# Optimization experiments

Hardware: AMD Instinct MI355X
Metric: run time of the kernel (lower is better)

## Reference

```python
import jax, jax.numpy as jnp
import numpy as np

B, N, D, H = 4, 2048, 1024, 16
HD = D // H          # head dim before LRPE doubling
CHUNK = 64
BASE = 10000.0
EPS = 1e-6


def setup_inputs() -> dict:
    key = jax.random.key(0)
    ks = jax.random.split(key, 8)
    s = 0.02
    return {
        "x": jax.random.normal(ks[0], (B, N, D), jnp.float32),
        "Wq": jax.random.normal(ks[1], (D, D), jnp.float32) * s,
        "Wk": jax.random.normal(ks[2], (D, D), jnp.float32) * s,
        "Wv": jax.random.normal(ks[3], (D, D), jnp.float32) * s,
        "Wo": jax.random.normal(ks[4], (D, D), jnp.float32) * s,
        "Wg1": jax.random.normal(ks[5], (D, H), jnp.float32) * s,
        "Wg2": jax.random.normal(ks[6], (H, D), jnp.float32) * s,
        "norm_w": jnp.ones((D,), jnp.float32),
    }


def _lrpe(x, theta):
    # cosine LRPE (lrpe_type=6): d -> 2d, concat([x*cos, x*sin])
    c = jnp.cos(theta)[None, :, None, :]
    s = jnp.sin(theta)[None, :, None, :]
    return jnp.concatenate([x * c, x * s], axis=-1)


def _chunk_gla(q, k, v, g):
    # GLA chunked scan: S_t = diag(exp(g_t)) S_{t-1} + k_t^T v_t ; o_t = q_t S_t
    # q,k,g: (b,n,h,dk), v: (b,n,h,dv)
    b, n, h, dk = q.shape
    dv = v.shape[-1]
    nc = n // CHUNK

    def to_chunks(t):
        return t.reshape(b, nc, CHUNK, t.shape[2], t.shape[3]).transpose(1, 0, 2, 3, 4)

    qc, kc, vc, gc = map(to_chunks, (q, k, v, g))  # (nc,b,C,h,*)
    mask = jnp.tril(jnp.ones((CHUNK, CHUNK), bool))

    def step(S, inp):
        qi, ki, vi, gi = inp                      # (b,C,h,dk/dv)
        G = jnp.cumsum(gi, axis=1)                # inclusive cumsum of log decay
        q_g = qi * jnp.exp(G)
        k_g = ki * jnp.exp(-G)
        o_inter = jnp.einsum('bchk,bhkv->bchv', q_g, S)
        A = jnp.einsum('bchk,bshk->bhcs', q_g, k_g)
        A = jnp.where(mask[None, None], A, 0.0)
        o_intra = jnp.einsum('bhcs,bshv->bchv', A, vi)
        G_last = G[:, -1:]                        # (b,1,h,dk)
        S = S * jnp.exp(G_last[:, 0])[..., None] + jnp.einsum(
            'bchk,bchv->bhkv', ki * jnp.exp(G_last - G), vi)
        return S, o_inter + o_intra

    S0 = jnp.zeros((b, h, dk, dv), q.dtype)
    _, o = jax.lax.scan(step, S0, (qc, kc, vc, gc))
    return o.transpose(1, 0, 2, 3, 4).reshape(b, n, h, dv)


def reference(x, Wq, Wk, Wv, Wo, Wg1, Wg2, norm_w):
    b, n, d = x.shape
    q = jax.nn.silu(x @ Wq).reshape(b, n, H, HD)
    k_raw = (x @ Wk).reshape(b, n, H, HD)
    v = (x @ Wv).reshape(b, n, H, HD)

    # log-space cumulative decay from raw k projection (scalar_decay=False path)
    f = jnp.concatenate([jnp.zeros((b, 1, H, HD), jnp.float32),
                         k_raw.astype(jnp.float32)], axis=1)
    z = jax.lax.cumlogsumexp(f, axis=1)           # (b,n+1,H,HD)
    log_f = z[:, :-1] - z[:, 1:]                  # per-step log decay (<=0)
    k = jnp.exp(k_raw - z[:, 1:])                 # normalized keys

    # cosine LRPE: angles (n,HD), doubles head dim
    theta = jnp.arange(n, dtype=jnp.float32)[:, None] * \
        (BASE ** (-2.0 * jnp.arange(HD, dtype=jnp.float32) / HD))[None]
    q = _lrpe(q, theta)
    k = _lrpe(k, theta)
    g = jnp.concatenate([log_f, log_f], axis=-1)  # repeat '... d -> ... (2 d)'

    o = _chunk_gla(q, k, v, g)                    # (b,n,H,HD)
    o = o.reshape(b, n, d)

    gate = jax.nn.sigmoid((x @ Wg1) @ Wg2)        # low-rank output gate
    o = o * gate
    o = o * jax.lax.rsqrt(jnp.mean(o * o, axis=-1, keepdims=True) + EPS) * norm_w
    return o @ Wo
```

## Files before the change

kernel.cpp:

```cpp
#include <hip/hip_runtime.h>
#include <hip/hip_bf16.h>
#include <math.h>

#define B_ 4
#define N_ 2048
#define D_ 1024
#define H_ 16
#define HD_ 64

typedef __attribute__((ext_vector_type(8))) short bf16x8;
typedef __attribute__((ext_vector_type(8))) unsigned short u16x8;
typedef __attribute__((ext_vector_type(4))) float f32x4;

#define AS1(p) ((const __attribute__((address_space(1))) void*)(p))
#define AS3(p) ((__attribute__((address_space(3))) void*)(p))

__device__ inline float bf2f(unsigned short u) { return __uint_as_float(((unsigned)u) << 16); }
__device__ inline unsigned short f2bf(float f) {
  unsigned u = __float_as_uint(f);
  return (unsigned short)((u + 0x7fffu + ((u >> 16) & 1u)) >> 16);
}
__device__ inline unsigned short f2h(float f) {
  _Float16 h = (_Float16)f; unsigned short u; __builtin_memcpy(&u, &h, 2); return u;
}
__device__ inline float h2f(unsigned short u) {
  _Float16 h; __builtin_memcpy(&h, &u, 2); return (float)h;
}
__device__ inline float lseop_fast(float a, float b) {
  float mx = fmaxf(a, b), mn = fminf(a, b);
  return mx + __logf(1.f + __expf(mn - mx));
}

__global__ __launch_bounds__(256) void cast_x_bf16(const float* __restrict__ x,
                                                   unsigned short* __restrict__ xb) {
  const int t = blockIdx.x * 256 + threadIdx.x;
  float4 a = ((const float4*)x)[(size_t)t * 2];
  float4 b = ((const float4*)x)[(size_t)t * 2 + 1];
  union { unsigned short u[8]; uint4 q; } pk;
  pk.u[0] = f2bf(a.x); pk.u[1] = f2bf(a.y); pk.u[2] = f2bf(a.z); pk.u[3] = f2bf(a.w);
  pk.u[4] = f2bf(b.x); pk.u[5] = f2bf(b.y); pk.u[6] = f2bf(b.z); pk.u[7] = f2bf(b.w);
  ((uint4*)xb)[t] = pk.q;
}

__global__ __launch_bounds__(256) void cast_w_all(
    const float* __restrict__ Wq, const float* __restrict__ Wk,
    const float* __restrict__ Wv, const float* __restrict__ Wo,
    unsigned short* __restrict__ Wqkv_p, unsigned short* __restrict__ Wo_p) {
  const int bid = blockIdx.x;
  const int which = bid >> 9;
  const float* W = (which == 0) ? Wq : (which == 1) ? Wk : (which == 2) ? Wv : Wo;
  const int col0 = (which == 1) ? 1024 : (which == 2) ? 2048 : 0;
  const int Ntot = (which == 3) ? 1024 : 3072;
  unsigned short* dst = (which == 3) ? Wo_p : Wqkv_p;
  const int t = (bid & 511) * 256 + threadIdx.x;
  const int kg = t >> 10, n = t & 1023;
  union { unsigned short u[8]; uint4 q; } pk;
#pragma unroll
  for (int r = 0; r < 8; ++r)
    pk.u[r] = f2bf(W[(size_t)(kg * 8 + r) * 1024 + n]);
  *(uint4*)&dst[((size_t)kg * Ntot + col0 + n) * 8] = pk.q;
}

__global__ __launch_bounds__(256) void pack_wg1(const float* __restrict__ Wg1,
                                                unsigned short* __restrict__ Wp) {
  const int t = blockIdx.x * 256 + threadIdx.x;
  const int kg = t >> 4, hh = t & 15;
  union { unsigned short us[8]; u16x8 v; } pk;
#pragma unroll
  for (int r = 0; r < 8; ++r)
    pk.us[r] = f2bf(Wg1[(size_t)(kg * 8 + r) * 16 + hh]);
  *(u16x8*)&Wp[((size_t)kg * 16 + hh) * 8] = pk.v;
}

__global__ __launch_bounds__(256) void gate_logits(
    const unsigned short* __restrict__ x_bf, const unsigned short* __restrict__ Wg1p,
    float* __restrict__ tg) {
  __shared__ unsigned short Wl[128 * 16 * 8];
  const int tid = threadIdx.x;
  const int lane = tid & 63, w = tid >> 6;
  const int lr = lane & 15, lg = lane >> 4;
#pragma unroll
  for (int u = 0; u < 8; ++u) {
    const int flat = u * 256 + tid;
    *(u16x8*)&Wl[flat * 8] = *(const u16x8*)&Wg1p[(size_t)flat * 8];
  }
  __syncthreads();
  const int row = blockIdx.x * 64 + w * 16 + lr;
  f32x4 acc = (f32x4){0.f, 0.f, 0.f, 0.f};
  for (int ks = 0; ks < 32; ++ks) {
    bf16x8 a = *(const bf16x8*)&x_bf[(size_t)row * 1024 + ks * 32 + lg * 8];
    bf16x8 b = *(const bf16x8*)&Wl[((ks * 4 + lg) * 16 + lr) * 8];
    acc = __builtin_amdgcn_mfma_f32_16x16x32_bf16(a, b, acc, 0, 0, 0);
  }
  const int orow = blockIdx.x * 64 + w * 16 + 4 * lg;
#pragma unroll
  for (int reg = 0; reg < 4; ++reg)
    tg[(size_t)(orow + reg) * 16 + lr] = acc[reg];
}

__global__ __launch_bounds__(256) void rope_fill(float* __restrict__ ropeT) {
  const int t = blockIdx.x * 256 + threadIdx.x;
  const int n = t >> 6, hd = t & 63;
  const float freq = expf((float)hd * -0.28782313662425575f);
  float s, c;
  sincosf((float)n * freq, &s, &c);
  ropeT[(size_t)n * 128 + hd] = c;
  ropeT[(size_t)n * 128 + 64 + hd] = s;
}

__global__ __launch_bounds__(256) void gemm_qkv(
    const unsigned short* __restrict__ A, const unsigned short* __restrict__ Wp,
    unsigned short* __restrict__ qb, unsigned short* __restrict__ kh,
    unsigned short* __restrict__ vb, float* __restrict__ T, int M, int K) {
  const int Nn = 3072;
  __shared__ unsigned short Asm[2][128 * 32];
  __shared__ unsigned short Bsm[2][4 * 128 * 8];

  const int tid = threadIdx.x;
  const int lane = tid & 63;
  const int w = tid >> 6;
  const int nb = Nn >> 7;
  const int nwg = gridDim.x;
  const int cpx = nwg >> 3;
  int bid = blockIdx.x;
  bid = (bid & 7) * cpx + (bid >> 3);
  const int by = bid / nb, bx = bid % nb;
  const int m0 = by * 128, n0 = bx * 128;
  const int wr = w >> 1, wc = w & 1;

  f32x4 acc[4][4];
#pragma unroll
  for (int i = 0; i < 4; ++i)
#pragma unroll
    for (int j = 0; j < 4; ++j) acc[i][j] = (f32x4){0.f, 0.f, 0.f, 0.f};

  const int rA0 = w * 16 + (lane >> 2);
  const int rA1 = (w + 4) * 16 + (lane >> 2);
  const int sA0 = (lane & 3) ^ ((rA0 >> 1) & 3);
  const int sA1 = (lane & 3) ^ ((rA1 >> 1) & 3);
  const unsigned short* gA0 = A + (size_t)(m0 + rA0) * K + sA0 * 8;
  const unsigned short* gA1 = A + (size_t)(m0 + rA1) * K + sA1 * 8;
  const unsigned short* gB0 = Wp + (size_t)(w >> 1) * Nn * 8 +
                              (size_t)(n0 + (w & 1) * 64 + lane) * 8;
  const unsigned short* gB1 = Wp + (size_t)((w + 4) >> 1) * Nn * 8 +
                              (size_t)(n0 + ((w + 4) & 1) * 64 + lane) * 8;

  int offA[4], offB[4];
#pragma unroll
  for (int m = 0; m < 4; ++m) {
    const int rowf = wr * 64 + m * 16 + (lane & 15);
    const int sp = (lane >> 4) ^ ((rowf >> 1) & 3);
    offA[m] = rowf * 32 + sp * 8;
  }
#pragma unroll
  for (int n = 0; n < 4; ++n) {
    const int colf = wc * 64 + n * 16 + (lane & 15);
    offB[n] = (lane >> 4) * 1024 + colf * 8;
  }

  auto STAGE = [&](int buf, int t) {
    const int kt = t * 32;
    const size_t kB = (size_t)(kt >> 3) * Nn * 8;
    __builtin_amdgcn_global_load_lds(AS1(gA0 + kt), AS3(&Asm[buf][w * 512]), 16, 0, 0);
    __builtin_amdgcn_global_load_lds(AS1(gA1 + kt), AS3(&Asm[buf][(w + 4) * 512]), 16, 0, 0);
    __builtin_amdgcn_global_load_lds(AS1(gB0 + kB), AS3(&Bsm[buf][w * 512]), 16, 0, 0);
    __builtin_amdgcn_global_load_lds(AS1(gB1 + kB), AS3(&Bsm[buf][(w + 4) * 512]), 16, 0, 0);
  };

  const int NT = K >> 5;
  STAGE(0, 0);
  __syncthreads();
  int cur = 0;
  for (int t = 0; t < NT; ++t) {
    if (t + 1 < NT) STAGE(cur ^ 1, t + 1);
    bf16x8 af[4], bfr[4];
#pragma unroll
    for (int m = 0; m < 4; ++m) af[m] = *(const bf16x8*)&Asm[cur][offA[m]];
#pragma unroll
    for (int n = 0; n < 4; ++n) bfr[n] = *(const bf16x8*)&Bsm[cur][offB[n]];
#pragma unroll
    for (int m = 0; m < 4; ++m)
#pragma unroll
      for (int n = 0; n < 4; ++n)
        acc[m][n] = __builtin_amdgcn_mfma_f32_16x16x32_bf16(af[m], bfr[n], acc[m][n], 0, 0, 0);
    __syncthreads();
    cur ^= 1;
  }

  const int crow = (lane >> 4) * 4;
  const int ccol = lane & 15;
  const int slice = bx >> 3;
  if (slice == 1) {
#pragma unroll
    for (int n = 0; n < 4; ++n) {
      float se = 0.f;
#pragma unroll
      for (int m = 0; m < 4; ++m)
#pragma unroll
        for (int r = 0; r < 4; ++r) {
          float vv = acc[m][n][r];
          se += __expf(vv);
          kh[(size_t)(m0 + wr * 64 + m * 16 + crow + r) * 1024 +
             (n0 & 1023) + wc * 64 + n * 16 + ccol] = f2h(vv);
        }
      se += __shfl_xor(se, 16);
      se += __shfl_xor(se, 32);
      if ((lane >> 4) == 0) {
        const int bb = m0 >> 11;
        const int h = ((n0 & 1023) + wc * 64) >> 6;
        const int hd = n * 16 + ccol;
        const int c = ((m0 & 2047) >> 6) + wr;
        T[(size_t)((bb * 16 + h) * 64 + hd) * 32 + c] = __logf(se);
      }
    }
  } else {
#pragma unroll
    for (int m = 0; m < 4; ++m)
#pragma unroll
      for (int n = 0; n < 4; ++n)
#pragma unroll
        for (int r = 0; r < 4; ++r) {
          float vv = acc[m][n][r];
          const size_t idx = (size_t)(m0 + wr * 64 + m * 16 + crow + r) * 1024 +
                             (n0 & 1023) + wc * 64 + n * 16 + ccol;
          if (slice == 0) {
            vv = vv / (1.f + __expf(-vv));
            qb[idx] = f2bf(vv);
          } else {
            vb[idx] = f2bf(vv);
          }
        }
  }
}

__global__ __launch_bounds__(256) void gemm_bf16(
    const unsigned short* __restrict__ A, const unsigned short* __restrict__ Wp,
    float* __restrict__ Cf, int M, int K, int Nn) {
  __shared__ unsigned short Asm[2][128 * 32];
  __shared__ unsigned short Bsm[2][4 * 128 * 8];

  const int tid = threadIdx.x;
  const int lane = tid & 63;
  const int w = tid >> 6;
  const int nb = Nn >> 7;
  const int nwg = gridDim.x;
  const int cpx = nwg >> 3;
  int bid = blockIdx.x;
  bid = (bid & 7) * cpx + (bid >> 3);
  const int by = bid / nb, bx = bid % nb;
  const int m0 = by * 128, n0 = bx * 128;
  const int wr = w >> 1, wc = w & 1;

  f32x4 acc[4][4];
#pragma unroll
  for (int i = 0; i < 4; ++i)
#pragma unroll
    for (int j = 0; j < 4; ++j) acc[i][j] = (f32x4){0.f, 0.f, 0.f, 0.f};

  const int rA0 = w * 16 + (lane >> 2);
  const int rA1 = (w + 4) * 16 + (lane >> 2);
  const int sA0 = (lane & 3) ^ ((rA0 >> 1) & 3);
  const int sA1 = (lane & 3) ^ ((rA1 >> 1) & 3);
  const unsigned short* gA0 = A + (size_t)(m0 + rA0) * K + sA0 * 8;
  const unsigned short* gA1 = A + (size_t)(m0 + rA1) * K + sA1 * 8;
  const unsigned short* gB0 = Wp + (size_t)(w >> 1) * Nn * 8 +
                              (size_t)(n0 + (w & 1) * 64 + lane) * 8;
  const unsigned short* gB1 = Wp + (size_t)((w + 4) >> 1) * Nn * 8 +
                              (size_t)(n0 + ((w + 4) & 1) * 64 + lane) * 8;

  int offA[4], offB[4];
#pragma unroll
  for (int m = 0; m < 4; ++m) {
    const int rowf = wr * 64 + m * 16 + (lane & 15);
    const int sp = (lane >> 4) ^ ((rowf >> 1) & 3);
    offA[m] = rowf * 32 + sp * 8;
  }
#pragma unroll
  for (int n = 0; n < 4; ++n) {
    const int colf = wc * 64 + n * 16 + (lane & 15);
    offB[n] = (lane >> 4) * 1024 + colf * 8;
  }

  auto STAGE = [&](int buf, int t) {
    const int kt = t * 32;
    const size_t kB = (size_t)(kt >> 3) * Nn * 8;
    __builtin_amdgcn_global_load_lds(AS1(gA0 + kt), AS3(&Asm[buf][w * 512]), 16, 0, 0);
    __builtin_amdgcn_global_load_lds(AS1(gA1 + kt), AS3(&Asm[buf][(w + 4) * 512]), 16, 0, 0);
    __builtin_amdgcn_global_load_lds(AS1(gB0 + kB), AS3(&Bsm[buf][w * 512]), 16, 0, 0);
    __builtin_amdgcn_global_load_lds(AS1(gB1 + kB), AS3(&Bsm[buf][(w + 4) * 512]), 16, 0, 0);
  };

  const int NT = K >> 5;
  STAGE(0, 0);
  __syncthreads();
  int cur = 0;
  for (int t = 0; t < NT; ++t) {
    if (t + 1 < NT) STAGE(cur ^ 1, t + 1);
    bf16x8 af[4], bfr[4];
#pragma unroll
    for (int m = 0; m < 4; ++m) af[m] = *(const bf16x8*)&Asm[cur][offA[m]];
#pragma unroll
    for (int n = 0; n < 4; ++n) bfr[n] = *(const bf16x8*)&Bsm[cur][offB[n]];
#pragma unroll
    for (int m = 0; m < 4; ++m)
#pragma unroll
      for (int n = 0; n < 4; ++n)
        acc[m][n] = __builtin_amdgcn_mfma_f32_16x16x32_bf16(af[m], bfr[n], acc[m][n], 0, 0, 0);
    __syncthreads();
    cur ^= 1;
  }

  const int crow = (lane >> 4) * 4;
  const int ccol = lane & 15;
#pragma unroll
  for (int m = 0; m < 4; ++m)
#pragma unroll
    for (int n = 0; n < 4; ++n) {
#pragma unroll
      for (int r = 0; r < 4; ++r) {
        Cf[(size_t)(m0 + wr * 64 + m * 16 + crow + r) * Nn +
           n0 + wc * 64 + n * 16 + ccol] = acc[m][n][r];
      }
    }
}

__global__ void scan_pass_b(const float* __restrict__ T, float* __restrict__ Pf) {
  const int ch = blockIdx.x * 256 + threadIdx.x;
  const float* t = &T[(size_t)ch * 32];
  float* p = &Pf[(size_t)ch * 32];
  float run = 0.f;
  for (int c = 0; c < 32; ++c) {
    p[c] = run;
    run = lseop_fast(run, t[c]);
  }
}

__global__ __launch_bounds__(256) void scan_pass_c(const unsigned short* __restrict__ k_h,
    const float* __restrict__ Pf, const float* __restrict__ ropeT,
    unsigned short* __restrict__ G_h, unsigned short* __restrict__ kg_g,
    float* __restrict__ glast_g) {
  const int g = blockIdx.x * 256 + threadIdx.x;
  const int hd = g & 63;
  const int c = (g >> 6) & 31;
  const int bh = g >> 11;
  const int b = bh >> 4, h = bh & 15;
  const size_t base = (size_t)b * N_ * D_ + (size_t)(c * 64) * D_ + h * HD_ + hd;
  const size_t gb = ((size_t)bh * N_ + c * 64) * 64 + hd;
  const size_t kb = ((size_t)bh * N_ + c * 64) * 128 + hd;
  const size_t rb = (size_t)(c * 64) * 128 + hd;
  const float P = Pf[(size_t)(bh * 64 + hd) * 32 + c];
  float S = 0.f, G = 0.f;
  for (int j0 = 0; j0 < 64; j0 += 8) {
    float kr[8], cv[8], sv[8];
#pragma unroll
    for (int e = 0; e < 8; ++e) kr[e] = h2f(k_h[base + (size_t)(j0 + e) * D_]);
#pragma unroll
    for (int e = 0; e < 8; ++e) {
      cv[e] = ropeT[rb + (size_t)(j0 + e) * 128];
      sv[e] = ropeT[rb + (size_t)(j0 + e) * 128 + 64];
    }
#pragma unroll
    for (int e = 0; e < 8; ++e) {
      float ei = __expf(kr[e] - P);
      S += ei;
      G = -__logf(1.f + S);
      G_h[gb + (size_t)(j0 + e) * 64] = f2h(G);
      kg_g[kb + (size_t)(j0 + e) * 128] = f2bf(ei * cv[e]);
      kg_g[kb + (size_t)(j0 + e) * 128 + 64] = f2bf(ei * sv[e]);
    }
  }
  glast_g[(size_t)(bh * 32 + c) * 64 + hd] = G;
}

__global__ __launch_bounds__(256) void gla_a(
    const unsigned short* __restrict__ qs, const unsigned short* __restrict__ kg_g,
    const unsigned short* __restrict__ G_h, const unsigned short* __restrict__ v_bf,
    const float* __restrict__ ropeT, const float* __restrict__ glast_g,
    unsigned short* __restrict__ qg_p, unsigned short* __restrict__ U,
    unsigned short* __restrict__ o_bf) {
  __shared__ unsigned short kg_l[64 * 128];
  __shared__ unsigned short kgT_l[128 * 72];
  __shared__ unsigned short vT_l[64 * 72];
  __shared__ unsigned short A_l[64 * 72];

  const int bid = blockIdx.x;
  const int bh = bid >> 5, c = bid & 31;
  const int b = bh >> 4, h = bh & 15;
  const int t0 = c * 64;
  const int tid = threadIdx.x;
  const int lane = tid & 63, w = tid >> 6;
  const int lr = lane & 15, lg = lane >> 4;

  const size_t qv_base = ((size_t)(b * N_ + t0) * H_ + h) * 64;
  const size_t kg_base = ((size_t)bh * N_ + t0) * 128;

#pragma unroll
  for (int u = 0; u < 4; ++u) {
    const int flat = u * 256 + tid;
    const int r = flat >> 4, sl = flat & 15;
    u16x8 src = *(const u16x8*)&kg_g[kg_base + (size_t)r * 128 + sl * 8];
    *(u16x8*)&kg_l[r * 128 + ((sl ^ (r & 7)) * 8)] = src;
  }
  {
    const int r = tid >> 2, d0 = (tid & 3) * 16;
    u16x8 a = *(const u16x8*)&v_bf[qv_base + (size_t)r * (H_ * 64) + d0];
    u16x8 b2 = *(const u16x8*)&v_bf[qv_base + (size_t)r * (H_ * 64) + d0 + 8];
#pragma unroll
    for (int e = 0; e < 8; ++e) {
      vT_l[(d0 + e) * 72 + r] = a[e];
      vT_l[(d0 + 8 + e) * 72 + r] = b2[e];
    }
  }
  __syncthreads();
  {
    const int j = tid >> 1, sh = (tid & 1) * 32;
#pragma unroll
    for (int u = 0; u < 4; ++u) {
      union { unsigned short us[8]; u16x8 v; } tv;
#pragma unroll
      for (int e = 0; e < 8; ++e) {
        const int s = sh + 8 * u + e;
        tv.us[e] = kg_l[s * 128 + (((j >> 3) ^ (s & 7)) * 8) + (j & 7)];
      }
      *(u16x8*)&kgT_l[j * 72 + sh + 8 * u] = tv.v;
    }
  }
  __syncthreads();

  bf16x8 af[4];
  {
    const int r = 16 * w + lr;
#pragma unroll
    for (int ks = 0; ks < 4; ++ks) {
      const int jb = 32 * ks + 8 * lg;
      const int jq = jb & 63;
      u16x8 q8 = *(const u16x8*)&qs[qv_base + (size_t)r * (H_ * 64) + jq];
      u16x8 gh8 = *(const u16x8*)&G_h[((size_t)bh * N_ + t0 + r) * 64 + jq];
      float4 r0 = *(const float4*)&ropeT[(size_t)(t0 + r) * 128 + jb];
      float4 r1 = *(const float4*)&ropeT[(size_t)(t0 + r) * 128 + jb + 4];
      float rr[8] = {r0.x, r0.y, r0.z, r0.w, r1.x, r1.y, r1.z, r1.w};
      union { unsigned short us[8]; bf16x8 v; u16x8 uv; } pk;
#pragma unroll
      for (int e = 0; e < 8; ++e)
        pk.us[e] = f2bf(bf2f(q8[e]) * rr[e] * __expf(h2f(gh8[e])));
      af[ks] = pk.v;
      *(u16x8*)&qg_p[((((size_t)bid * 4 + w) * 4 + ks) * 64 + lane) * 8] = pk.uv;
    }
  }
  f32x4 acc1[4];
#pragma unroll
  for (int n = 0; n < 4; ++n) acc1[n] = (f32x4){0.f, 0.f, 0.f, 0.f};
#pragma unroll
  for (int n = 0; n < 4; ++n) {
    const int s = 16 * n + lr;
#pragma unroll
    for (int ks = 0; ks < 4; ++ks) {
      bf16x8 bk = *(const bf16x8*)&kg_l[s * 128 + (((lg + 4 * ks) ^ (s & 7)) * 8)];
      acc1[n] = __builtin_amdgcn_mfma_f32_16x16x32_bf16(af[ks], bk, acc1[n], 0, 0, 0);
    }
  }
#pragma unroll
  for (int n = 0; n < 4; ++n) {
    const int s = 16 * n + lr;
#pragma unroll
    for (int reg = 0; reg < 4; ++reg) {
      const int cr = 16 * w + 4 * lg + reg;
      A_l[cr * 72 + s] = (s <= cr) ? f2bf(acc1[n][reg]) : (unsigned short)0;
    }
  }
  f32x4 acc2[8];
#pragma unroll
  for (int n = 0; n < 8; ++n) acc2[n] = (f32x4){0.f, 0.f, 0.f, 0.f};
#pragma unroll
  for (int ks = 0; ks < 2; ++ks) {
    const int s0 = 32 * ks + 8 * lg;
    bf16x8 av = *(const bf16x8*)&vT_l[(16 * w + lr) * 72 + s0];
#pragma unroll
    for (int n = 0; n < 8; ++n) {
      bf16x8 bk = *(const bf16x8*)&kgT_l[(16 * n + lr) * 72 + s0];
      acc2[n] = __builtin_amdgcn_mfma_f32_16x16x32_bf16(av, bk, acc2[n], 0, 0, 0);
    }
  }
  __syncthreads();
  float es[4];
#pragma unroll
  for (int n = 0; n < 4; ++n)
    es[n] = __expf(glast_g[(size_t)bid * 64 + 16 * n + lr]);
#pragma unroll
  for (int n = 0; n < 8; ++n) {
    const int j = 16 * n + lr;
    const float e = es[n & 3];
#pragma unroll
    for (int reg = 0; reg < 4; ++reg)
      kg_l[(16 * w + 4 * lg + reg) * 128 + j] = f2bf(acc2[n][reg] * e);
  }
  f32x4 acc3[4];
#pragma unroll
  for (int n = 0; n < 4; ++n) acc3[n] = (f32x4){0.f, 0.f, 0.f, 0.f};
#pragma unroll
  for (int ks = 0; ks < 2; ++ks) {
    const int s0 = 32 * ks + 8 * lg;
    bf16x8 aA = *(const bf16x8*)&A_l[(16 * w + lr) * 72 + s0];
#pragma unroll
    for (int n = 0; n < 4; ++n) {
      bf16x8 bV = *(const bf16x8*)&vT_l[(16 * n + lr) * 72 + s0];
      acc3[n] = __builtin_amdgcn_mfma_f32_16x16x32_bf16(aA, bV, acc3[n], 0, 0, 0);
    }
  }
#pragma unroll
  for (int n = 0; n < 4; ++n)
#pragma unroll
    for (int reg = 0; reg < 4; ++reg)
      o_bf[qv_base + (size_t)(16 * w + 4 * lg + reg) * (H_ * 64) + 16 * n + lr] =
          f2bf(acc3[n][reg]);
  __syncthreads();
#pragma unroll
  for (int u = 0; u < 4; ++u) {
    const int flat = u * 256 + tid;
    const int d = flat >> 4, sl = flat & 15;
    *(u16x8*)&U[((size_t)bid * 64 + d) * 128 + sl * 8] =
        *(const u16x8*)&kg_l[d * 128 + sl * 8];
  }
}

__global__ __launch_bounds__(256) void gla_b(unsigned short* __restrict__ U,
                                             const float* __restrict__ glast_g) {
  const int t = blockIdx.x * 256 + threadIdx.x;
  const int j4 = t & 31;
  const int d = (t >> 5) & 63;
  const int bh = t >> 11;
  const int jj0 = (4 * j4) & 63;
  float s0 = 0.f, s1 = 0.f, s2 = 0.f, s3 = 0.f;
  for (int c = 0; c < 32; ++c) {
    const size_t ub = ((size_t)((bh * 32 + c) * 64 + d)) * 128 + 4 * j4;
    ushort4 uv = *(const ushort4*)&U[ub];
    float4 g4 = *(const float4*)&glast_g[(size_t)(bh * 32 + c) * 64 + jj0];
    ushort4 pv;
    pv.x = f2bf(s0); pv.y = f2bf(s1); pv.z = f2bf(s2); pv.w = f2bf(s3);
    *(ushort4*)&U[ub] = pv;
    s0 = s0 * __expf(g4.x) + bf2f(uv.x);
    s1 = s1 * __expf(g4.y) + bf2f(uv.y);
    s2 = s2 * __expf(g4.z) + bf2f(uv.z);
    s3 = s3 * __expf(g4.w) + bf2f(uv.w);
  }
}

__global__ __launch_bounds__(256) void gla_c(
    const unsigned short* __restrict__ qg_p, const unsigned short* __restrict__ S,
    unsigned short* __restrict__ o_bf) {
  __shared__ unsigned short S_l[64 * 128];
  const int bid = blockIdx.x;
  const int bh = bid >> 5, c = bid & 31;
  const int b = bh >> 4, h = bh & 15;
  const int t0 = c * 64;
  const int tid = threadIdx.x;
  const int lane = tid & 63, w = tid >> 6;
  const int lr = lane & 15, lg = lane >> 4;
  const size_t s_base = (size_t)bid * 64 * 128;
  const size_t o_base = ((size_t)(b * N_ + t0) * H_ + h) * 64;

#pragma unroll
  for (int u = 0; u < 4; ++u) {
    const int flat = u * 256 + tid;
    const int d = flat >> 4, sl = flat & 15;
    u16x8 src = *(const u16x8*)&S[s_base + (size_t)d * 128 + sl * 8];
    *(u16x8*)&S_l[d * 128 + ((sl ^ (d & 7)) * 8)] = src;
  }
  __syncthreads();
  bf16x8 af[4];
#pragma unroll
  for (int ks = 0; ks < 4; ++ks)
    af[ks] = *(const bf16x8*)&qg_p[((((size_t)bid * 4 + w) * 4 + ks) * 64 + lane) * 8];
  f32x4 acc[4];
#pragma unroll
  for (int n = 0; n < 4; ++n) acc[n] = (f32x4){0.f, 0.f, 0.f, 0.f};
#pragma unroll
  for (int n = 0; n < 4; ++n) {
    const int d = 16 * n + lr;
#pragma unroll
    for (int ks = 0; ks < 4; ++ks) {
      bf16x8 bk = *(const bf16x8*)&S_l[d * 128 + (((lg + 4 * ks) ^ (d & 7)) * 8)];
      acc[n] = __builtin_amdgcn_mfma_f32_16x16x32_bf16(af[ks], bk, acc[n], 0, 0, 0);
    }
  }
#pragma unroll
  for (int n = 0; n < 4; ++n)
#pragma unroll
    for (int reg = 0; reg < 4; ++reg) {
      const size_t idx = o_base + (size_t)(16 * w + 4 * lg + reg) * (H_ * 64) + 16 * n + lr;
      o_bf[idx] = f2bf(bf2f(o_bf[idx]) + acc[n][reg]);
    }
}

__global__ __launch_bounds__(256) void gate_norm2(
    const float* __restrict__ tg, const float* __restrict__ Wg2,
    const float* __restrict__ nw, const unsigned short* __restrict__ o_bf,
    unsigned short* __restrict__ og) {
  const int w = threadIdx.x >> 6, lane = threadIdx.x & 63;
  const int row = blockIdx.x * 4 + w;
  float tgv[16];
  const float* tp = &tg[(size_t)row * 16];
#pragma unroll
  for (int hh = 0; hh < 16; ++hh) tgv[hh] = tp[hh];
  float ogr[4][4];
  float ssq = 0.f;
#pragma unroll
  for (int u = 0; u < 4; ++u) {
    const int d0 = u * 256 + lane * 4;
    ushort4 o4 = *(const ushort4*)&o_bf[(size_t)row * 1024 + d0];
    float oa[4] = {bf2f(o4.x), bf2f(o4.y), bf2f(o4.z), bf2f(o4.w)};
    float sgx = 0.f, sgy = 0.f, sgz = 0.f, sgw = 0.f;
#pragma unroll
    for (int hh = 0; hh < 16; ++hh) {
      float4 w4 = *(const float4*)&Wg2[hh * 1024 + d0];
      sgx += tgv[hh] * w4.x; sgy += tgv[hh] * w4.y;
      sgz += tgv[hh] * w4.z; sgw += tgv[hh] * w4.w;
    }
    ogr[u][0] = oa[0] / (1.f + __expf(-sgx));
    ogr[u][1] = oa[1] / (1.f + __expf(-sgy));
    ogr[u][2] = oa[2] / (1.f + __expf(-sgz));
    ogr[u][3] = oa[3] / (1.f + __expf(-sgw));
    ssq += ogr[u][0] * ogr[u][0] + ogr[u][1] * ogr[u][1] +
           ogr[u][2] * ogr[u][2] + ogr[u][3] * ogr[u][3];
  }
#pragma unroll
  for (int off = 32; off > 0; off >>= 1) ssq += __shfl_xor(ssq, off);
  const float rinv = rsqrtf(ssq * (1.f / 1024.f) + 1e-6f);
#pragma unroll
  for (int u = 0; u < 4; ++u) {
    const int d0 = u * 256 + lane * 4;
    float4 nw4 = *(const float4*)&nw[d0];
    ushort4 st;
    st.x = f2bf(ogr[u][0] * rinv * nw4.x);
    st.y = f2bf(ogr[u][1] * rinv * nw4.y);
    st.z = f2bf(ogr[u][2] * rinv * nw4.z);
    st.w = f2bf(ogr[u][3] * rinv * nw4.w);
    *(ushort4*)&og[(size_t)row * 1024 + d0] = st;
  }
}

extern "C" void kernel_launch(void* const* d_in, const int* in_sizes, int n_in,
                              void* d_out, int out_size, void* d_ws, size_t ws_size,
                              hipStream_t stream) {
  const float* x   = (const float*)d_in[0];
  const float* Wq  = (const float*)d_in[1];
  const float* Wk  = (const float*)d_in[2];
  const float* Wv  = (const float*)d_in[3];
  const float* Wo  = (const float*)d_in[4];
  const float* Wg1 = (const float*)d_in[5];
  const float* Wg2 = (const float*)d_in[6];
  const float* nw  = (const float*)d_in[7];
  float* out = (float*)d_out;
  float* ws  = (float*)d_ws;

  const size_t P = (size_t)B_ * N_ * D_;
  unsigned short* k_h = (unsigned short*)ws;
  unsigned short* U_buf = (unsigned short*)ws;
  unsigned short* o_bf = (unsigned short*)(ws + P);
  unsigned short* G_h  = (unsigned short*)(ws + 2 * P);
  unsigned short* qg_p = (unsigned short*)(ws + 3 * P);
  unsigned short* kg_g = (unsigned short*)(ws + 4 * P);
  unsigned short* v_bf = (unsigned short*)(ws + 5 * P);
  unsigned short* q_bf = (unsigned short*)(ws + 5 * P + P / 2);
  float* ropeT = ws + 6 * P;
  float* T_buf = ws + 6 * P + 524288;
  float* P_buf = T_buf + 131072;
  unsigned short* Wg1p = (unsigned short*)(ws + 6 * P + 786432);
  float* tg_buf = ws + 6 * P + 794624;
  unsigned short* x_bf = (unsigned short*)(ws + 13 * P / 2);
  unsigned short* og_bf = x_bf;
  unsigned short* Wqkv_p = (unsigned short*)(ws + 7 * P);
  unsigned short* Wo_p = (unsigned short*)(ws + 7 * P + 1572864);
  float* glast_g = ws + 7 * P + 2097152;

  const int M = B_ * N_;
  const int ggrid = (M / 128) * (D_ / 128);
  const int qkvgrid = (M / 128) * (3 * D_ / 128);

  cast_x_bf16<<<(int)(P / 2048), 256, 0, stream>>>(x, x_bf);
  rope_fill<<<512, 256, 0, stream>>>(ropeT);
  cast_w_all<<<2048, 256, 0, stream>>>(Wq, Wk, Wv, Wo, Wqkv_p, Wo_p);
  pack_wg1<<<8, 256, 0, stream>>>(Wg1, Wg1p);
  gate_logits<<<M / 64, 256, 0, stream>>>(x_bf, Wg1p, tg_buf);
  gemm_qkv<<<qkvgrid, 256, 0, stream>>>(x_bf, Wqkv_p, q_bf, k_h, v_bf, T_buf, M, D_);
  scan_pass_b<<<16, 256, 0, stream>>>(T_buf, P_buf);
  scan_pass_c<<<512, 256, 0, stream>>>(k_h, P_buf, ropeT, G_h, kg_g, glast_g);
  gla_a<<<2048, 256, 0, stream>>>(q_bf, kg_g, G_h, v_bf, ropeT, glast_g, qg_p, U_buf, o_bf);
  gla_b<<<512, 256, 0, stream>>>(U_buf, glast_g);
  gla_c<<<2048, 256, 0, stream>>>(qg_p, U_buf, o_bf);
  gate_norm2<<<M / 4, 256, 0, stream>>>(tg_buf, Wg2, nw, o_bf, og_bf);
  gemm_bf16<<<ggrid, 256, 0, stream>>>(og_bf, Wo_p, out, M, D_, D_);
}
```

Measured before the change: 229.9 us.

## Fuse intra-chunk decay scan and key normalization into gla_a

Removes the separate scan_pass_c kernel and computes normalized keys, LRPE-rotated k_g, the cumulative log-decay G, and the chunk-last decay inside gla_a using shared memory. A four-way split of each 64-row chunk does partial sums that are combined through shared totals. This avoids writing and re-reading the G_h and kg_g global buffers and saves one kernel launch. The cost is extra LDS use (G_l, tot_l, glast_s), which may lower occupancy of gla_a, and uncoalesced strided k_h reads. U_buf is moved to a separate workspace region so it no longer aliases k_h, which gla_a now reads while writing U.

```diff
diff --git a/kernel.cpp b/kernel.cpp
--- a/kernel.cpp
+++ b/kernel.cpp
@@ -335,53 +335,19 @@
   }
 }
 
-__global__ __launch_bounds__(256) void scan_pass_c(const unsigned short* __restrict__ k_h,
-    const float* __restrict__ Pf, const float* __restrict__ ropeT,
-    unsigned short* __restrict__ G_h, unsigned short* __restrict__ kg_g,
-    float* __restrict__ glast_g) {
-  const int g = blockIdx.x * 256 + threadIdx.x;
-  const int hd = g & 63;
-  const int c = (g >> 6) & 31;
-  const int bh = g >> 11;
-  const int b = bh >> 4, h = bh & 15;
-  const size_t base = (size_t)b * N_ * D_ + (size_t)(c * 64) * D_ + h * HD_ + hd;
-  const size_t gb = ((size_t)bh * N_ + c * 64) * 64 + hd;
-  const size_t kb = ((size_t)bh * N_ + c * 64) * 128 + hd;
-  const size_t rb = (size_t)(c * 64) * 128 + hd;
-  const float P = Pf[(size_t)(bh * 64 + hd) * 32 + c];
-  float S = 0.f, G = 0.f;
-  for (int j0 = 0; j0 < 64; j0 += 8) {
-    float kr[8], cv[8], sv[8];
-#pragma unroll
-    for (int e = 0; e < 8; ++e) kr[e] = h2f(k_h[base + (size_t)(j0 + e) * D_]);
-#pragma unroll
-    for (int e = 0; e < 8; ++e) {
-      cv[e] = ropeT[rb + (size_t)(j0 + e) * 128];
-      sv[e] = ropeT[rb + (size_t)(j0 + e) * 128 + 64];
-    }
-#pragma unroll
-    for (int e = 0; e < 8; ++e) {
-      float ei = __expf(kr[e] - P);
-      S += ei;
-      G = -__logf(1.f + S);
-      G_h[gb + (size_t)(j0 + e) * 64] = f2h(G);
-      kg_g[kb + (size_t)(j0 + e) * 128] = f2bf(ei * cv[e]);
-      kg_g[kb + (size_t)(j0 + e) * 128 + 64] = f2bf(ei * sv[e]);
-    }
-  }
-  glast_g[(size_t)(bh * 32 + c) * 64 + hd] = G;
-}
-
 __global__ __launch_bounds__(256) void gla_a(
-    const unsigned short* __restrict__ qs, const unsigned short* __restrict__ kg_g,
-    const unsigned short* __restrict__ G_h, const unsigned short* __restrict__ v_bf,
-    const float* __restrict__ ropeT, const float* __restrict__ glast_g,
+    const unsigned short* __restrict__ qs, const unsigned short* __restrict__ k_h,
+    const float* __restrict__ Pf, const unsigned short* __restrict__ v_bf,
+    const float* __restrict__ ropeT,
     unsigned short* __restrict__ qg_p, unsigned short* __restrict__ U,
-    unsigned short* __restrict__ o_bf) {
+    unsigned short* __restrict__ o_bf, float* __restrict__ glast_g) {
   __shared__ unsigned short kg_l[64 * 128];
   __shared__ unsigned short kgT_l[128 * 72];
   __shared__ unsigned short vT_l[64 * 72];
   __shared__ unsigned short A_l[64 * 72];
+  __shared__ unsigned short G_l[64 * 72];
+  __shared__ float tot_l[4][64];
+  __shared__ float glast_s[64];
 
   const int bid = blockIdx.x;
   const int bh = bid >> 5, c = bid & 31;
@@ -392,35 +358,60 @@
   const int lr = lane & 15, lg = lane >> 4;
 
   const size_t qv_base = ((size_t)(b * N_ + t0) * H_ + h) * 64;
-  const size_t kg_base = ((size_t)bh * N_ + t0) * 128;
-
-#pragma unroll
-  for (int u = 0; u < 4; ++u) {
-    const int flat = u * 256 + tid;
-    const int r = flat >> 4, sl = flat & 15;
-    u16x8 src = *(const u16x8*)&kg_g[kg_base + (size_t)r * 128 + sl * 8];
-    *(u16x8*)&kg_l[r * 128 + ((sl ^ (r & 7)) * 8)] = src;
+
+  const int jch = tid & 63, qq = tid >> 6;
+  float e[16];
+  {
+    const float P = Pf[((size_t)bh * 64 + jch) * 32 + c];
+    float psum = 0.f;
+#pragma unroll
+    for (int i = 0; i < 16; ++i) {
+      const int r = qq * 16 + i;
+      float kv = h2f(k_h[qv_base + (size_t)r * 1024 + jch]);
+      float ei = __expf(kv - P);
+      e[i] = ei;
+      psum += ei;
+      float cv = ropeT[(size_t)(t0 + r) * 128 + jch];
+      float sv = ropeT[(size_t)(t0 + r) * 128 + 64 + jch];
+      kg_l[r * 128 + (((jch >> 3) ^ (r & 7)) << 3) + (jch & 7)] = f2bf(ei * cv);
+      kg_l[r * 128 + ((((jch + 64) >> 3) ^ (r & 7)) << 3) + (jch & 7)] = f2bf(ei * sv);
+    }
+    tot_l[qq][jch] = psum;
   }
   {
     const int r = tid >> 2, d0 = (tid & 3) * 16;
     u16x8 a = *(const u16x8*)&v_bf[qv_base + (size_t)r * (H_ * 64) + d0];
     u16x8 b2 = *(const u16x8*)&v_bf[qv_base + (size_t)r * (H_ * 64) + d0 + 8];
 #pragma unroll
-    for (int e = 0; e < 8; ++e) {
-      vT_l[(d0 + e) * 72 + r] = a[e];
-      vT_l[(d0 + 8 + e) * 72 + r] = b2[e];
-    }
-  }
-  __syncthreads();
+    for (int ee = 0; ee < 8; ++ee) {
+      vT_l[(d0 + ee) * 72 + r] = a[ee];
+      vT_l[(d0 + 8 + ee) * 72 + r] = b2[ee];
+    }
+  }
+  __syncthreads();
+  {
+    float off = 0.f;
+    for (int p = 0; p < qq; ++p) off += tot_l[p][jch];
+    float S = off;
+#pragma unroll
+    for (int i = 0; i < 16; ++i) {
+      S += e[i];
+      G_l[(qq * 16 + i) * 72 + jch] = f2h(-__logf(1.f + S));
+    }
+    if (qq == 3) {
+      glast_g[(size_t)bid * 64 + jch] = -__logf(1.f + S);
+      glast_s[jch] = 1.f / (1.f + S);
+    }
+  }
   {
     const int j = tid >> 1, sh = (tid & 1) * 32;
 #pragma unroll
     for (int u = 0; u < 4; ++u) {
       union { unsigned short us[8]; u16x8 v; } tv;
 #pragma unroll
-      for (int e = 0; e < 8; ++e) {
-        const int s = sh + 8 * u + e;
-        tv.us[e] = kg_l[s * 128 + (((j >> 3) ^ (s & 7)) * 8) + (j & 7)];
+      for (int ee = 0; ee < 8; ++ee) {
+        const int s = sh + 8 * u + ee;
+        tv.us[ee] = kg_l[s * 128 + (((j >> 3) ^ (s & 7)) * 8) + (j & 7)];
       }
       *(u16x8*)&kgT_l[j * 72 + sh + 8 * u] = tv.v;
     }
@@ -435,14 +426,14 @@
       const int jb = 32 * ks + 8 * lg;
       const int jq = jb & 63;
       u16x8 q8 = *(const u16x8*)&qs[qv_base + (size_t)r * (H_ * 64) + jq];
-      u16x8 gh8 = *(const u16x8*)&G_h[((size_t)bh * N_ + t0 + r) * 64 + jq];
+      u16x8 gh8 = *(const u16x8*)&G_l[r * 72 + jq];
       float4 r0 = *(const float4*)&ropeT[(size_t)(t0 + r) * 128 + jb];
       float4 r1 = *(const float4*)&ropeT[(size_t)(t0 + r) * 128 + jb + 4];
       float rr[8] = {r0.x, r0.y, r0.z, r0.w, r1.x, r1.y, r1.z, r1.w};
       union { unsigned short us[8]; bf16x8 v; u16x8 uv; } pk;
 #pragma unroll
-      for (int e = 0; e < 8; ++e)
-        pk.us[e] = f2bf(bf2f(q8[e]) * rr[e] * __expf(h2f(gh8[e])));
+      for (int ee = 0; ee < 8; ++ee)
+        pk.us[ee] = f2bf(bf2f(q8[ee]) * rr[ee] * __expf(h2f(gh8[ee])));
       af[ks] = pk.v;
       *(u16x8*)&qg_p[((((size_t)bid * 4 + w) * 4 + ks) * 64 + lane) * 8] = pk.uv;
     }
@@ -484,15 +475,14 @@
   __syncthreads();
   float es[4];
 #pragma unroll
-  for (int n = 0; n < 4; ++n)
-    es[n] = __expf(glast_g[(size_t)bid * 64 + 16 * n + lr]);
+  for (int n = 0; n < 4; ++n) es[n] = glast_s[16 * n + lr];
 #pragma unroll
   for (int n = 0; n < 8; ++n) {
     const int j = 16 * n + lr;
-    const float e = es[n & 3];
+    const float ee = es[n & 3];
 #pragma unroll
     for (int reg = 0; reg < 4; ++reg)
-      kg_l[(16 * w + 4 * lg + reg) * 128 + j] = f2bf(acc2[n][reg] * e);
+      kg_l[(16 * w + 4 * lg + reg) * 128 + j] = f2bf(acc2[n][reg] * ee);
   }
   f32x4 acc3[4];
 #pragma unroll
@@ -655,11 +645,9 @@
 
   const size_t P = (size_t)B_ * N_ * D_;
   unsigned short* k_h = (unsigned short*)ws;
-  unsigned short* U_buf = (unsigned short*)ws;
   unsigned short* o_bf = (unsigned short*)(ws + P);
-  unsigned short* G_h  = (unsigned short*)(ws + 2 * P);
   unsigned short* qg_p = (unsigned short*)(ws + 3 * P);
-  unsigned short* kg_g = (unsigned short*)(ws + 4 * P);
+  unsigned short* U_buf = (unsigned short*)(ws + 4 * P);
   unsigned short* v_bf = (unsigned short*)(ws + 5 * P);
   unsigned short* q_bf = (unsigned short*)(ws + 5 * P + P / 2);
   float* ropeT = ws + 6 * P;
@@ -684,8 +672,7 @@
   gate_logits<<<M / 64, 256, 0, stream>>>(x_bf, Wg1p, tg_buf);
   gemm_qkv<<<qkvgrid, 256, 0, stream>>>(x_bf, Wqkv_p, q_bf, k_h, v_bf, T_buf, M, D_);
   scan_pass_b<<<16, 256, 0, stream>>>(T_buf, P_buf);
-  scan_pass_c<<<512, 256, 0, stream>>>(k_h, P_buf, ropeT, G_h, kg_g, glast_g);
-  gla_a<<<2048, 256, 0, stream>>>(q_bf, kg_g, G_h, v_bf, ropeT, glast_g, qg_p, U_buf, o_bf);
+  gla_a<<<2048, 256, 0, stream>>>(q_bf, k_h, P_buf, v_bf, ropeT, qg_p, U_buf, o_bf, glast_g);
   gla_b<<<512, 256, 0, stream>>>(U_buf, glast_g);
   gla_c<<<2048, 256, 0, stream>>>(qg_p, U_buf, o_bf);
   gate_norm2<<<M / 4, 256, 0, stream>>>(tg_buf, Wg2, nw, o_bf, og_bf);
```

Result: faster. 214.9 us (-6.5%).
